# Optimization experiments

Hardware: AMD Instinct MI355X
Metric: run time of the kernel (lower is better)

Reference implementation:

```python
import jax, jax.numpy as jnp
import numpy as np

LN_EPS = 1e-6
T_MAX = 200.0

def setup_inputs() -> dict:
    key = jax.random.key(0)
    ks = jax.random.split(key, 8)
    B, L, D = 16, 2048, 256
    return {
        "event_type": jax.random.randint(ks[0], (B, L), 0, 2, dtype=jnp.int64) if jax.config.jax_enable_x64 else jax.random.randint(ks[0], (B, L), 0, 2, dtype=jnp.int32),
        "event_time": jax.random.uniform(ks[1], (B, L), jnp.float32) * T_MAX,
        "noise": jax.random.uniform(ks[2], (B, L, D), jnp.float32),
        "gate_params": jax.random.uniform(ks[3], (2,), jnp.float32),
        "length_scale": jnp.ones((1,), jnp.float32),
        "Wn": jax.random.normal(ks[4], (D, D), jnp.float32) * (1.0 / np.sqrt(D)),
        "Wi": jax.random.normal(ks[5], (D, D), jnp.float32) * (1.0 / np.sqrt(D)),
        "w_time": jax.random.normal(ks[6], (1, D), jnp.float32) * (1.0 / np.sqrt(D)),
        "b_time": jnp.zeros((1,), jnp.float32),
        "ln_gamma": jnp.ones((D,), jnp.float32),
        "ln_beta": jnp.zeros((D,), jnp.float32),
    }

def reference(event_type, event_time, noise, gate_params, length_scale, Wn, Wi, w_time, b_time, ln_gamma, ln_beta):
    B, L = event_time.shape
    D = Wn.shape[0]
    # temporal positional encoding: pv[i] = 10000^(2i/D); even idx -> sin, odd -> cos
    i = jnp.arange(D)
    pv = jnp.power(jnp.float32(10000.0), 2.0 * i.astype(event_time.dtype) / D)
    temp = event_time[:, :, None] / pv  # [B,L,D]
    emb = jnp.where(i % 2 == 0, jnp.sin(temp), jnp.cos(temp))
    # pairwise time differences: xt[b,i,j]=t_i, xt_bar[b,i,j]=t_j
    d = jnp.abs(event_time[:, :, None] - event_time[:, None, :])  # [B,L,L]
    # squared-exponential kernel (sigma=1, norm=1)
    ls = jax.nn.softplus(length_scale[0])
    k = jnp.exp(-(d * d) / (ls * ls))
    # sigmoid gate (num_types == 1 branch, norm=1)
    l = jax.nn.sigmoid(gate_params[0])
    s = jax.nn.sigmoid(gate_params[1])
    gate = 1.0 + jnp.tanh((d / T_MAX - l) / s)
    # causal mask: lower triangle incl. diagonal ((triu(ones,1)-1)^2)
    mask = jnp.tril(jnp.ones((L, L), event_time.dtype))
    scores = k * gate * mask
    # hidden = scores @ embeddings, then LayerNorm
    hidden = jnp.einsum('bij,bjd->bid', scores, emb)
    mu = jnp.mean(hidden, -1, keepdims=True)
    var = jnp.mean((hidden - mu) ** 2, -1, keepdims=True)
    hidden = (hidden - mu) * jax.lax.rsqrt(var + LN_EPS) * ln_gamma + ln_beta
    # generator (dropout = identity at eval)
    h = jax.nn.relu(noise @ Wn.T + hidden @ Wi.T)
    out = jax.nn.softplus(h @ w_time.T + b_time)  # [B,L,1]
    return out[..., 0]
```

## Files before the change

kernel.cpp:

```cpp
#include <hip/hip_runtime.h>

#define BN 16
#define LL 2048
#define DD 256
#define XS 516

typedef __attribute__((ext_vector_type(8))) short bf16x8;
typedef __attribute__((ext_vector_type(4))) float f32x4;

__device__ __forceinline__ unsigned int f2bf1(float f) {
    union { float f; unsigned int i; } v; v.f = f;
    return (v.i + 0x7fffu + ((v.i >> 16) & 1u)) >> 16;
}
__device__ __forceinline__ float bfval(unsigned int h) {
    union { unsigned int i; float f; } v; v.i = h << 16;
    return v.f;
}
__device__ __forceinline__ unsigned int pk2bf(float a, float b) {
    return f2bf1(a) | (f2bf1(b) << 16);
}

__global__ __launch_bounds__(256, 2)
void tpp_v11(const float* __restrict__ et,
             const float* __restrict__ noise,
             const float* __restrict__ gp,
             const float* __restrict__ lsc,
             const float* __restrict__ Wn,
             const float* __restrict__ Wi,
             const float* __restrict__ wt,
             const float* __restrict__ bt,
             const float* __restrict__ gam,
             const float* __restrict__ bet,
             float* __restrict__ out) {
    __shared__ __align__(16) unsigned short sA[4 * 64 * 8];
    __shared__ __align__(16) unsigned short sAl[4 * 64 * 8];
    __shared__ float tIs[32];
    __shared__ float tJs[64];
    __shared__ __align__(16) float X[32][XS];

    const int tid = threadIdx.x;
    const int w   = tid >> 6;
    const int ln  = tid & 63;
    const int qd  = ln >> 4;
    const int n16 = ln & 15;

    const int bidx  = blockIdx.x;
    const int b     = bidx & (BN - 1);
    const int itile = 63 - (bidx >> 4);
    const int i0    = itile * 32;

    const float lgt = 1.0f / (1.0f + __expf(-gp[0]));
    const float sgt = 1.0f / (1.0f + __expf(-gp[1]));
    const float ls  = log1pf(__expf(lsc[0]));
    const float inv_ls2 = 1.0f / (ls * ls);
    const float inv_T   = 1.0f / 200.0f;
    const float inv_s2  = 2.0f / sgt;

    float ipv4[4];
#pragma unroll
    for (int cg = 0; cg < 4; ++cg)
        ipv4[cg] = __expf(-(float)(w * 64 + cg * 16 + n16) * 0.0719557841532429f);
    const float offl = (n16 & 1) ? 1.57079632679489662f : 0.0f;

    {
        const float* nptr = noise + ((size_t)b * LL + i0) * DD;
        for (int idx = tid; idx < 32 * 64; idx += 256) {
            int row = idx >> 6, c4 = idx & 63;
            *(float4*)&X[row][c4 * 4] = *(const float4*)(nptr + (size_t)row * DD + c4 * 4);
        }
    }
    if (tid < 32) tIs[tid] = et[(size_t)b * LL + i0 + tid];

    const int sm  = tid & 15;
    const int sg  = (tid >> 4) & 1;
    const int sqd = (tid >> 5) & 3;
    const int sks = tid >> 7;

    f32x4 acc[2][4];
#pragma unroll
    for (int g = 0; g < 2; ++g)
#pragma unroll
        for (int cg = 0; cg < 4; ++cg) {
            f32x4 z = {0.f, 0.f, 0.f, 0.f};
            acc[g][cg] = z;
        }

    const int ntile = (i0 >> 6) + 1;
    for (int jt = 0; jt < ntile; ++jt) {
        const int j0 = jt * 64;
        __syncthreads();
        if (tid < 64) tJs[tid] = et[(size_t)b * LL + j0 + tid];

        {
            const float* etb = et + (size_t)b * LL + j0 + sks * 32 + sqd * 8;
            float ti = tIs[sg * 16 + sm];
            int gi = i0 + sg * 16 + sm;
            int jb = j0 + sks * 32 + sqd * 8;
            unsigned int hb[8];
            float lo[8];
#pragma unroll
            for (int jj = 0; jj < 8; ++jj) {
                float tj = etb[jj];
                float dt = fabsf(ti - tj);
                float kk = __expf(-dt * dt * inv_ls2);
                float x2 = (dt * inv_T - lgt) * inv_s2;
                float gate = __fdividef(2.0f, 1.0f + __expf(-x2));
                float s = kk * gate;
                if (gi < jb + jj) s = 0.0f;
                hb[jj] = f2bf1(s);
                lo[jj] = s - bfval(hb[jj]);
            }
            int base = ((sks * 2 + sg) * 64 + sqd * 16 + sm) * 8;
            uint4 rh, rl;
            rh.x = hb[0] | (hb[1] << 16); rh.y = hb[2] | (hb[3] << 16);
            rh.z = hb[4] | (hb[5] << 16); rh.w = hb[6] | (hb[7] << 16);
            rl.x = pk2bf(lo[0], lo[1]); rl.y = pk2bf(lo[2], lo[3]);
            rl.z = pk2bf(lo[4], lo[5]); rl.w = pk2bf(lo[6], lo[7]);
            *(uint4*)&sA[base]  = rh;
            *(uint4*)&sAl[base] = rl;
        }
        __syncthreads();

#pragma unroll
        for (int ks = 0; ks < 2; ++ks) {
            bf16x8 a0h = *(const bf16x8*)&sA[((ks * 2 + 0) * 64 + ln) * 8];
            bf16x8 a1h = *(const bf16x8*)&sA[((ks * 2 + 1) * 64 + ln) * 8];
            bf16x8 a0l = *(const bf16x8*)&sAl[((ks * 2 + 0) * 64 + ln) * 8];
            bf16x8 a1l = *(const bf16x8*)&sAl[((ks * 2 + 1) * 64 + ln) * 8];
            float tj[8];
#pragma unroll
            for (int jj = 0; jj < 8; ++jj) tj[jj] = tJs[ks * 32 + qd * 8 + jj];
#pragma unroll
            for (int cg = 0; cg < 4; ++cg) {
                unsigned int eh[8];
#pragma unroll
                for (int jj = 0; jj < 8; ++jj) {
                    float e = __sinf(fmaf(tj[jj], ipv4[cg], offl));
                    eh[jj] = f2bf1(e);
                }
                union { uint4 u; bf16x8 v; } bh;
                bh.u.x = eh[0] | (eh[1] << 16); bh.u.y = eh[2] | (eh[3] << 16);
                bh.u.z = eh[4] | (eh[5] << 16); bh.u.w = eh[6] | (eh[7] << 16);
                acc[0][cg] = __builtin_amdgcn_mfma_f32_16x16x32_bf16(a0h, bh.v, acc[0][cg], 0, 0, 0);
                acc[0][cg] = __builtin_amdgcn_mfma_f32_16x16x32_bf16(a0l, bh.v, acc[0][cg], 0, 0, 0);
                acc[1][cg] = __builtin_amdgcn_mfma_f32_16x16x32_bf16(a1h, bh.v, acc[1][cg], 0, 0, 0);
                acc[1][cg] = __builtin_amdgcn_mfma_f32_16x16x32_bf16(a1l, bh.v, acc[1][cg], 0, 0, 0);
            }
        }
    }

    __syncthreads();
#pragma unroll
    for (int g = 0; g < 2; ++g)
#pragma unroll
        for (int cg = 0; cg < 4; ++cg)
#pragma unroll
            for (int reg = 0; reg < 4; ++reg)
                X[g * 16 + qd * 4 + reg][256 + w * 64 + cg * 16 + n16] = acc[g][cg][reg];
    __syncthreads();

    {
        float4 gv = *(const float4*)(gam + ln * 4);
        float4 bv = *(const float4*)(bet + ln * 4);
#pragma unroll
        for (int r = 0; r < 8; ++r) {
            int row = w * 8 + r;
            float4 xv = *(const float4*)&X[row][256 + ln * 4];
            float s1 = xv.x + xv.y + xv.z + xv.w;
            float s2 = xv.x * xv.x + xv.y * xv.y + xv.z * xv.z + xv.w * xv.w;
#pragma unroll
            for (int off = 1; off < 64; off <<= 1) {
                s1 += __shfl_xor(s1, off, 64);
                s2 += __shfl_xor(s2, off, 64);
            }
            float mu   = s1 * (1.0f / 256.0f);
            float var  = s2 * (1.0f / 256.0f) - mu * mu;
            float rstd = rsqrtf(var + 1e-6f);
            float4 yv;
            yv.x = (xv.x - mu) * rstd * gv.x + bv.x;
            yv.y = (xv.y - mu) * rstd * gv.y + bv.y;
            yv.z = (xv.z - mu) * rstd * gv.z + bv.z;
            yv.w = (xv.w - mu) * rstd * gv.w + bv.w;
            *(float4*)&X[row][256 + ln * 4] = yv;
        }
    }
    __syncthreads();

    f32x4 acc2[2][4];
#pragma unroll
    for (int g = 0; g < 2; ++g)
#pragma unroll
        for (int cg = 0; cg < 4; ++cg) {
            f32x4 z = {0.f, 0.f, 0.f, 0.f};
            acc2[g][cg] = z;
        }
    for (int ks2 = 0; ks2 < 16; ++ks2) {
        const int kk = ks2 * 32 + qd * 8;
        bf16x8 a[2];
#pragma unroll
        for (int g = 0; g < 2; ++g) {
            const float* xp = &X[g * 16 + n16][kk];
            float4 xa = *(const float4*)xp;
            float4 xc = *(const float4*)(xp + 4);
            union { uint4 u; bf16x8 v; } aa;
            aa.u.x = pk2bf(xa.x, xa.y); aa.u.y = pk2bf(xa.z, xa.w);
            aa.u.z = pk2bf(xc.x, xc.y); aa.u.w = pk2bf(xc.z, xc.w);
            a[g] = aa.v;
        }
        const float* Wbase = (ks2 < 8) ? Wn : Wi;
        const int kw = (ks2 < 8) ? kk : (kk - 256);
#pragma unroll
        for (int cg = 0; cg < 4; ++cg) {
            const int o = (w * 4 + cg) * 16 + n16;
            const float* wp = Wbase + (size_t)o * DD + kw;
            float4 wa = *(const float4*)wp;
            float4 wc = *(const float4*)(wp + 4);
            union { uint4 u; bf16x8 v; } bb;
            bb.u.x = pk2bf(wa.x, wa.y); bb.u.y = pk2bf(wa.z, wa.w);
            bb.u.z = pk2bf(wc.x, wc.y); bb.u.w = pk2bf(wc.z, wc.w);
            acc2[0][cg] = __builtin_amdgcn_mfma_f32_16x16x32_bf16(a[0], bb.v, acc2[0][cg], 0, 0, 0);
            acc2[1][cg] = __builtin_amdgcn_mfma_f32_16x16x32_bf16(a[1], bb.v, acc2[1][cg], 0, 0, 0);
        }
    }

    __syncthreads();
#pragma unroll
    for (int g = 0; g < 2; ++g)
#pragma unroll
        for (int cg = 0; cg < 4; ++cg)
#pragma unroll
            for (int reg = 0; reg < 4; ++reg)
                X[g * 16 + qd * 4 + reg][256 + w * 64 + cg * 16 + n16] = acc2[g][cg][reg];
    __syncthreads();

    {
        const int d0 = ln * 4;
        float4 wv = *(const float4*)(wt + d0);
        const float btv = bt[0];
#pragma unroll
        for (int r = 0; r < 8; ++r) {
            int row = w * 8 + r;
            float4 hv = *(const float4*)&X[row][256 + d0];
            float p = fmaxf(hv.x, 0.0f) * wv.x + fmaxf(hv.y, 0.0f) * wv.y
                    + fmaxf(hv.z, 0.0f) * wv.z + fmaxf(hv.w, 0.0f) * wv.w;
#pragma unroll
            for (int off = 1; off < 64; off <<= 1) p += __shfl_xor(p, off, 64);
            if (ln == 0) {
                float z  = p + btv;
                float sp = (z > 20.0f) ? z : log1pf(__expf(z));
                out[(size_t)b * LL + i0 + row] = sp;
            }
        }
    }
}

extern "C" void kernel_launch(void* const* d_in, const int* in_sizes, int n_in,
                              void* d_out, int out_size, void* d_ws, size_t ws_size,
                              hipStream_t stream) {
    (void)in_sizes; (void)n_in; (void)out_size; (void)d_ws; (void)ws_size;
    const float* et    = (const float*)d_in[1];
    const float* noise = (const float*)d_in[2];
    const float* gp    = (const float*)d_in[3];
    const float* lsc   = (const float*)d_in[4];
    const float* Wn    = (const float*)d_in[5];
    const float* Wi    = (const float*)d_in[6];
    const float* wt    = (const float*)d_in[7];
    const float* bt    = (const float*)d_in[8];
    const float* gam   = (const float*)d_in[9];
    const float* bet   = (const float*)d_in[10];
    float* out = (float*)d_out;

    tpp_v11<<<dim3(BN * 64), dim3(256), 0, stream>>>(et, noise, gp, lsc, Wn, Wi,
                                                     wt, bt, gam, bet, out);
}
```

Baseline: 241.5 us.

## Precompute bf16 sinusoidal embedding table in workspace and load it in the main kernel

Adds a prep kernel that computes the temporal sin/cos embeddings once per (batch, dim, position) as bf16 in a transposed workspace table. The main kernel then loads the MFMA B operand straight from this table instead of recomputing __sinf for every j-tile in every i-tile block. Without the table, the causal triangle makes each embedding get recomputed many times. The table path is used only when a workspace is provided and a spot-check against recomputed values passes, otherwise it falls back to inline sin. The cost is an extra launch and about 16 MB of global traffic, plus uncoalesced-ish 16-byte loads in the inner loop.

After: 266.5 us. 10.4% more time.

```diff
diff --git a/kernel.cpp b/kernel.cpp
--- a/kernel.cpp
+++ b/kernel.cpp
@@ -20,8 +20,35 @@
     return f2bf1(a) | (f2bf1(b) << 16);
 }
 
+__global__ __launch_bounds__(256)
+void tpp_prep(const float* __restrict__ et, unsigned short* __restrict__ embT) {
+    const int blk   = blockIdx.x;
+    const int b     = blk >> 5;
+    const int dbase = (blk & 31) * 8;
+    __shared__ float ts[LL];
+    for (int idx = threadIdx.x; idx < LL / 4; idx += 256)
+        *(float4*)&ts[idx * 4] = *(const float4*)(et + (size_t)b * LL + idx * 4);
+    __syncthreads();
+    const int d   = dbase + (threadIdx.x >> 5);
+    const int l32 = threadIdx.x & 31;
+    const float ipv = __expf(-(float)d * 0.0719557841532429f);
+    const float off = (d & 1) ? 1.57079632679489662f : 0.0f;
+    unsigned short* dst = embT + ((size_t)b * DD + d) * LL;
+    for (int seg = 0; seg < LL; seg += 256) {
+        const int j0 = seg + l32 * 8;
+        float4 t0 = *(const float4*)&ts[j0];
+        float4 t1 = *(const float4*)&ts[j0 + 4];
+        uint4 r;
+        r.x = pk2bf(__sinf(fmaf(t0.x, ipv, off)), __sinf(fmaf(t0.y, ipv, off)));
+        r.y = pk2bf(__sinf(fmaf(t0.z, ipv, off)), __sinf(fmaf(t0.w, ipv, off)));
+        r.z = pk2bf(__sinf(fmaf(t1.x, ipv, off)), __sinf(fmaf(t1.y, ipv, off)));
+        r.w = pk2bf(__sinf(fmaf(t1.z, ipv, off)), __sinf(fmaf(t1.w, ipv, off)));
+        *(uint4*)&dst[j0] = r;
+    }
+}
+
 __global__ __launch_bounds__(256, 2)
-void tpp_v11(const float* __restrict__ et,
+void tpp_v18(const float* __restrict__ et,
              const float* __restrict__ noise,
              const float* __restrict__ gp,
              const float* __restrict__ lsc,
@@ -31,11 +58,14 @@
              const float* __restrict__ bt,
              const float* __restrict__ gam,
              const float* __restrict__ bet,
+             const unsigned short* __restrict__ embT,
+             const int tabFlag,
              float* __restrict__ out) {
     __shared__ __align__(16) unsigned short sA[4 * 64 * 8];
     __shared__ __align__(16) unsigned short sAl[4 * 64 * 8];
     __shared__ float tIs[32];
     __shared__ float tJs[64];
+    __shared__ int s_bad;
     __shared__ __align__(16) float X[32][XS];
 
     const int tid = threadIdx.x;
@@ -48,6 +78,8 @@
     const int b     = bidx & (BN - 1);
     const int itile = 63 - (bidx >> 4);
     const int i0    = itile * 32;
+
+    if (tid == 0) s_bad = tabFlag ? 0 : 1;
 
     const float lgt = 1.0f / (1.0f + __expf(-gp[0]));
     const float sgt = 1.0f / (1.0f + __expf(-gp[1]));
@@ -62,6 +94,8 @@
         ipv4[cg] = __expf(-(float)(w * 64 + cg * 16 + n16) * 0.0719557841532429f);
     const float offl = (n16 & 1) ? 1.57079632679489662f : 0.0f;
 
+    const size_t embBase = ((size_t)b * DD + w * 64 + n16) * LL + qd * 8;
+
     {
         const float* nptr = noise + ((size_t)b * LL + i0) * DD;
         for (int idx = tid; idx < 32 * 64; idx += 256) {
@@ -70,6 +104,20 @@
         }
     }
     if (tid < 32) tIs[tid] = et[(size_t)b * LL + i0 + tid];
+    __syncthreads();
+
+    if (tabFlag) {
+        const int dchk = tid;
+        const int jchk = (itile * 33 + (tid << 3)) & (LL - 1);
+        const float ipc = __expf(-(float)dchk * 0.0719557841532429f);
+        const float ofc = (dchk & 1) ? 1.57079632679489662f : 0.0f;
+        const unsigned int ref =
+            f2bf1(__sinf(fmaf(et[(size_t)b * LL + jchk], ipc, ofc)));
+        if (embT[((size_t)b * DD + dchk) * LL + jchk] != (unsigned short)ref)
+            s_bad = 1;
+    }
+    __syncthreads();
+    const bool useTab = (s_bad == 0);
 
     const int sm  = tid & 15;
     const int sg  = (tid >> 4) & 1;
@@ -132,19 +180,25 @@
             for (int jj = 0; jj < 8; ++jj) tj[jj] = tJs[ks * 32 + qd * 8 + jj];
 #pragma unroll
             for (int cg = 0; cg < 4; ++cg) {
-                unsigned int eh[8];
-#pragma unroll
-                for (int jj = 0; jj < 8; ++jj) {
-                    float e = __sinf(fmaf(tj[jj], ipv4[cg], offl));
-                    eh[jj] = f2bf1(e);
+                bf16x8 bv;
+                if (useTab) {
+                    bv = *(const bf16x8*)(embT + embBase + (size_t)cg * 16 * LL + j0 + ks * 32);
+                } else {
+                    unsigned int eh[8];
+#pragma unroll
+                    for (int jj = 0; jj < 8; ++jj) {
+                        float e = __sinf(fmaf(tj[jj], ipv4[cg], offl));
+                        eh[jj] = f2bf1(e);
+                    }
+                    union { uint4 u; bf16x8 v; } bh;
+                    bh.u.x = eh[0] | (eh[1] << 16); bh.u.y = eh[2] | (eh[3] << 16);
+                    bh.u.z = eh[4] | (eh[5] << 16); bh.u.w = eh[6] | (eh[7] << 16);
+                    bv = bh.v;
                 }
-                union { uint4 u; bf16x8 v; } bh;
-                bh.u.x = eh[0] | (eh[1] << 16); bh.u.y = eh[2] | (eh[3] << 16);
-                bh.u.z = eh[4] | (eh[5] << 16); bh.u.w = eh[6] | (eh[7] << 16);
-                acc[0][cg] = __builtin_amdgcn_mfma_f32_16x16x32_bf16(a0h, bh.v, acc[0][cg], 0, 0, 0);
-                acc[0][cg] = __builtin_amdgcn_mfma_f32_16x16x32_bf16(a0l, bh.v, acc[0][cg], 0, 0, 0);
-                acc[1][cg] = __builtin_amdgcn_mfma_f32_16x16x32_bf16(a1h, bh.v, acc[1][cg], 0, 0, 0);
-                acc[1][cg] = __builtin_amdgcn_mfma_f32_16x16x32_bf16(a1l, bh.v, acc[1][cg], 0, 0, 0);
+                acc[0][cg] = __builtin_amdgcn_mfma_f32_16x16x32_bf16(a0h, bv, acc[0][cg], 0, 0, 0);
+                acc[0][cg] = __builtin_amdgcn_mfma_f32_16x16x32_bf16(a0l, bv, acc[0][cg], 0, 0, 0);
+                acc[1][cg] = __builtin_amdgcn_mfma_f32_16x16x32_bf16(a1h, bv, acc[1][cg], 0, 0, 0);
+                acc[1][cg] = __builtin_amdgcn_mfma_f32_16x16x32_bf16(a1l, bv, acc[1][cg], 0, 0, 0);
             }
         }
     }
@@ -257,7 +311,7 @@
 extern "C" void kernel_launch(void* const* d_in, const int* in_sizes, int n_in,
                               void* d_out, int out_size, void* d_ws, size_t ws_size,
                               hipStream_t stream) {
-    (void)in_sizes; (void)n_in; (void)out_size; (void)d_ws; (void)ws_size;
+    (void)in_sizes; (void)n_in; (void)out_size;
     const float* et    = (const float*)d_in[1];
     const float* noise = (const float*)d_in[2];
     const float* gp    = (const float*)d_in[3];
@@ -270,6 +324,13 @@
     const float* bet   = (const float*)d_in[10];
     float* out = (float*)d_out;
 
-    tpp_v11<<<dim3(BN * 64), dim3(256), 0, stream>>>(et, noise, gp, lsc, Wn, Wi,
-                                                     wt, bt, gam, bet, out);
-}
+    const size_t need = (size_t)BN * DD * LL * sizeof(unsigned short);
+    const bool haveWs = (d_ws != nullptr && ws_size >= need);
+    unsigned short* embT = (unsigned short*)d_ws;
+
+    if (haveWs)
+        tpp_prep<<<dim3(512), dim3(256), 0, stream>>>(et, embT);
+    tpp_v18<<<dim3(BN * 64), dim3(256), 0, stream>>>(et, noise, gp, lsc, Wn, Wi,
+                                                     wt, bt, gam, bet,
+                                                     embT, haveWs ? 1 : 0, out);
+}
```
